# Kernel optimization log

Hardware: AMD Instinct MI355X
Metric: run time of the kernel (lower is better)

The kernel has to match this reference:

```python
import jax, jax.numpy as jnp
import numpy as np

B, S, D = 2, 2048, 2560
H, DH = 32, 80           # heads, head_size = D // H
RD = 32                  # rotary_dim (partial RoPE)
NI = 10240               # n_inner = 4 * n_embd
EPS = 1e-5
ROPE_BASE = 10000.0


def setup_inputs() -> dict:
    key = jax.random.key(0)
    ks = jax.random.split(key, 12)
    sd = 0.02
    inp = {
        "position_ids": jnp.broadcast_to(jnp.arange(S, dtype=jnp.int64), (B, S)),
        "hidden_states": jax.random.normal(ks[0], (B, S, D), jnp.float32),
        "ln_g": jnp.ones((D,), jnp.float32),
        "ln_b": jnp.zeros((D,), jnp.float32),
        "wqkv": jax.random.normal(ks[1], (D, 3 * D), jnp.float32) * sd,
        "bqkv": jnp.zeros((3 * D,), jnp.float32),
        "wout": jax.random.normal(ks[2], (D, D), jnp.float32) * sd,
        "bout": jnp.zeros((D,), jnp.float32),
        "wfc1": jax.random.normal(ks[3], (D, NI), jnp.float32) * sd,
        "bfc1": jnp.zeros((NI,), jnp.float32),
        "wfc2": jax.random.normal(ks[4], (NI, D), jnp.float32) * sd,
        "bfc2": jnp.zeros((D,), jnp.float32),
    }
    return inp


def _rope_neox(x, positions):
    # x: [B,S,H,DH]; apply neox-style rotary to first RD dims only
    half = RD // 2
    inv_freq = 1.0 / (ROPE_BASE ** (jnp.arange(0, RD, 2, dtype=jnp.float32) / RD))  # [half]
    ang = positions.astype(jnp.float32)[..., None] * inv_freq                        # [B,S,half]
    cos = jnp.cos(ang)[:, :, None, :]  # [B,S,1,half]
    sin = jnp.sin(ang)[:, :, None, :]
    x1 = x[..., :half]
    x2 = x[..., half:RD]
    rot = jnp.concatenate([x1 * cos - x2 * sin, x2 * cos + x1 * sin], axis=-1)
    return jnp.concatenate([rot, x[..., RD:]], axis=-1)


def reference(position_ids, hidden_states, ln_g, ln_b, wqkv, bqkv, wout, bout,
              wfc1, bfc1, wfc2, bfc2):
    residual = hidden_states
    # LayerNorm
    mu = jnp.mean(hidden_states, axis=-1, keepdims=True)
    var = jnp.mean(jnp.square(hidden_states - mu), axis=-1, keepdims=True)
    x = (hidden_states - mu) * jax.lax.rsqrt(var + EPS) * ln_g + ln_b

    # QKV projection
    qkv = x @ wqkv + bqkv
    q, k, v = jnp.split(qkv, 3, axis=-1)
    q = q.reshape(B, S, H, DH)
    k = k.reshape(B, S, H, DH)
    v = v.reshape(B, S, H, DH)

    # partial RoPE (neox style) on q and k
    q = _rope_neox(q, position_ids)
    k = _rope_neox(k, position_ids)

    # causal attention
    scale = DH ** -0.5
    scores = jnp.einsum("bqhd,bkhd->bhqk", q, k) * scale
    causal = jnp.tril(jnp.ones((S, S), jnp.bool_))
    scores = jnp.where(causal, scores, jnp.finfo(scores.dtype).min)
    probs = jax.nn.softmax(scores, axis=-1)
    attn = jnp.einsum("bhqk,bkhd->bqhd", probs, v).reshape(B, S, D)
    attn_out = attn @ wout + bout

    # MLP (gelu_new = tanh-approx gelu) on the SAME normed x (parallel residual)
    mlp = jax.nn.gelu(x @ wfc1 + bfc1, approximate=True) @ wfc2 + bfc2

    return attn_out + mlp + residual
```

## Files before the change

### kernel.cpp

```cpp
#include <hip/hip_runtime.h>

#define SS   2048
#define DD   2560
#define HH   32
#define DHH  80
#define DPAD 96
#define NII  10240
#define NTOK 4096

typedef __attribute__((ext_vector_type(8))) __bf16 bf16x8;
typedef __attribute__((ext_vector_type(4))) float  f32x4;

__device__ __forceinline__ float bf2f(unsigned short h) {
  union { unsigned u; float f; } c; c.u = ((unsigned)h) << 16; return c.f;
}
__device__ __forceinline__ unsigned short f2bf(float f) {
  union { float f; unsigned u; } c; c.f = f;
  unsigned r = c.u + 0x7FFFu + ((c.u >> 16) & 1u);
  return (unsigned short)(r >> 16);
}

__device__ __forceinline__ void gl_lds16(const void* gptr, void* lptr) {
  __builtin_amdgcn_global_load_lds((__attribute__((address_space(1))) void*)gptr,
                                   (__attribute__((address_space(3))) void*)lptr,
                                   16, 0, 0);
}

__global__ __launch_bounds__(256) void wt_transpose(const float* __restrict__ W,
                                                    unsigned short* __restrict__ Wt,
                                                    int K, int N) {
  __shared__ float tile[32][33];
  const int tx = threadIdx.x & 31, ty = threadIdx.x >> 5;
  const int n0 = blockIdx.x * 32, k0 = blockIdx.y * 32;
#pragma unroll
  for (int i = 0; i < 32; i += 8)
    tile[ty + i][tx] = W[(size_t)(k0 + ty + i) * N + n0 + tx];
  __syncthreads();
#pragma unroll
  for (int i = 0; i < 32; i += 8)
    Wt[(size_t)(n0 + ty + i) * K + k0 + tx] = f2bf(tile[tx][ty + i]);
}

__global__ __launch_bounds__(256) void ln_kernel(const float* __restrict__ X,
                                                 const float* __restrict__ G,
                                                 const float* __restrict__ Bb,
                                                 unsigned short* __restrict__ Xo) {
  const int row = blockIdx.x;
  const float4* xr = (const float4*)(X + (size_t)row * DD);
  float s = 0.f, ss = 0.f;
  for (int i = threadIdx.x; i < DD / 4; i += 256) {
    float4 v = xr[i];
    s  += v.x + v.y + v.z + v.w;
    ss += v.x * v.x + v.y * v.y + v.z * v.z + v.w * v.w;
  }
#pragma unroll
  for (int o = 32; o > 0; o >>= 1) { s += __shfl_down(s, o, 64); ss += __shfl_down(ss, o, 64); }
  __shared__ float red[8];
  const int w = threadIdx.x >> 6;
  if ((threadIdx.x & 63) == 0) { red[w] = s; red[4 + w] = ss; }
  __syncthreads();
  if (threadIdx.x == 0) {
    float ts  = red[0] + red[1] + red[2] + red[3];
    float tss = red[4] + red[5] + red[6] + red[7];
    float mu  = ts * (1.f / DD);
    float var = tss * (1.f / DD) - mu * mu;
    red[0] = mu; red[1] = rsqrtf(var + 1e-5f);
  }
  __syncthreads();
  const float mu = red[0], rstd = red[1];
  const float4* gr = (const float4*)G;
  const float4* br = (const float4*)Bb;
  for (int i = threadIdx.x; i < DD / 4; i += 256) {
    float4 v = xr[i], g = gr[i], b = br[i];
    ushort4 o;
    o.x = f2bf((v.x - mu) * rstd * g.x + b.x);
    o.y = f2bf((v.y - mu) * rstd * g.y + b.y);
    o.z = f2bf((v.z - mu) * rstd * g.z + b.z);
    o.w = f2bf((v.w - mu) * rstd * g.w + b.w);
    *(ushort4*)&Xo[(size_t)row * DD + i * 4] = o;
  }
}

__global__ __launch_bounds__(256) void rope_kernel(const unsigned short* __restrict__ qkv,
                                                   unsigned short* __restrict__ Qp,
                                                   unsigned short* __restrict__ Kp,
                                                   unsigned short* __restrict__ Vt) {
  const int tok = blockIdx.x;
  const int b = tok / SS, s = tok % SS;
  __shared__ float cs[16], sn[16];
  if (threadIdx.x < 16) {
    float inv = powf(10000.f, -(float)threadIdx.x / 16.f);
    float ang = (float)s * inv;
    cs[threadIdx.x] = cosf(ang);
    sn[threadIdx.x] = sinf(ang);
  }
  __syncthreads();
  const unsigned short* row = qkv + (size_t)tok * (3 * DD);
  for (int idx = threadIdx.x; idx < 2 * HH * DPAD; idx += 256) {
    const int which = idx / (HH * DPAD);
    const int rrem  = idx % (HH * DPAD);
    const int h = rrem / DPAD, d = rrem % DPAD;
    float val = 0.f;
    if (d < DHH) {
      const unsigned short* base = row + which * DD + h * DHH;
      if (d < 16) {
        float x1 = bf2f(base[d]), x2 = bf2f(base[d + 16]);
        val = x1 * cs[d] - x2 * sn[d];
      } else if (d < 32) {
        int i2 = d - 16;
        float x1 = bf2f(base[i2]), x2 = bf2f(base[d]);
        val = x2 * cs[i2] + x1 * sn[i2];
      } else {
        val = bf2f(base[d]);
      }
    }
    unsigned short* outp = which ? Kp : Qp;
    outp[(((size_t)b * HH + h) * SS + s) * DPAD + d] = f2bf(val);
  }
  for (int idx = threadIdx.x; idx < DD; idx += 256) {
    const int h = idx / DHH, d = idx % DHH;
    Vt[(((size_t)b * HH + h) * DHH + d) * SS + s] = row[2 * DD + idx];
  }
}

__global__ __launch_bounds__(128) void attn_kernel(const unsigned short* __restrict__ Qp,
                                                   const unsigned short* __restrict__ Kp,
                                                   const unsigned short* __restrict__ Vt,
                                                   unsigned short* __restrict__ O) {
  const int bid = blockIdx.x;
  const int bh = bid & 63;
  const int p = 63 - (bid >> 6);
  const int w = threadIdx.x >> 6;
  const int tile = p * 2 + w;
  const int lane = threadIdx.x & 63;
  const int lr = lane & 15, lg = lane >> 4;
  const int q0 = tile * 16;
  const unsigned short* Qh = Qp + (size_t)bh * SS * DPAD;
  const unsigned short* Kh = Kp + (size_t)bh * SS * DPAD;
  const unsigned short* Vh = Vt + (size_t)bh * DHH * SS;
  __shared__ __align__(16) char Plds[2][2048];
  char* Pb = Plds[w];

  bf16x8 qf[3];
#pragma unroll
  for (int c = 0; c < 3; ++c)
    qf[c] = *(const bf16x8*)&Qh[(size_t)(q0 + lr) * DPAD + c * 32 + lg * 8];

  f32x4 oacc[5];
#pragma unroll
  for (int d = 0; d < 5; ++d) oacc[d] = (f32x4){0.f, 0.f, 0.f, 0.f};
  float mrow[4], lrow[4];
#pragma unroll
  for (int r = 0; r < 4; ++r) { mrow[r] = -1e30f; lrow[r] = 0.f; }

  const float scl = 0.11180339887498949f;
  const int nt = q0 / 64 + 1;
  for (int t = 0; t < nt; ++t) {
    const int kv0 = t * 64;
    f32x4 s0 = (f32x4){0.f, 0.f, 0.f, 0.f};
    f32x4 s1 = (f32x4){0.f, 0.f, 0.f, 0.f};
    f32x4 s2 = (f32x4){0.f, 0.f, 0.f, 0.f};
    f32x4 s3 = (f32x4){0.f, 0.f, 0.f, 0.f};
#pragma unroll
    for (int c = 0; c < 3; ++c) {
      bf16x8 k0 = *(const bf16x8*)&Kh[(size_t)(kv0 +      lr) * DPAD + c * 32 + lg * 8];
      bf16x8 k1 = *(const bf16x8*)&Kh[(size_t)(kv0 + 16 + lr) * DPAD + c * 32 + lg * 8];
      bf16x8 k2 = *(const bf16x8*)&Kh[(size_t)(kv0 + 32 + lr) * DPAD + c * 32 + lg * 8];
      bf16x8 k3 = *(const bf16x8*)&Kh[(size_t)(kv0 + 48 + lr) * DPAD + c * 32 + lg * 8];
      s0 = __builtin_amdgcn_mfma_f32_16x16x32_bf16(qf[c], k0, s0, 0, 0, 0);
      s1 = __builtin_amdgcn_mfma_f32_16x16x32_bf16(qf[c], k1, s1, 0, 0, 0);
      s2 = __builtin_amdgcn_mfma_f32_16x16x32_bf16(qf[c], k2, s2, 0, 0, 0);
      s3 = __builtin_amdgcn_mfma_f32_16x16x32_bf16(qf[c], k3, s3, 0, 0, 0);
    }
    float pv0[4], pv1[4], pv2[4], pv3[4], mx[4];
    bool need = false;
#pragma unroll
    for (int r = 0; r < 4; ++r) {
      const int qr = q0 + lg * 4 + r;
      float a0 = (kv0 +      lr > qr) ? -1e30f : s0[r] * scl;
      float a1 = (kv0 + 16 + lr > qr) ? -1e30f : s1[r] * scl;
      float a2 = (kv0 + 32 + lr > qr) ? -1e30f : s2[r] * scl;
      float a3 = (kv0 + 48 + lr > qr) ? -1e30f : s3[r] * scl;
      pv0[r] = a0; pv1[r] = a1; pv2[r] = a2; pv3[r] = a3;
      float m = fmaxf(fmaxf(a0, a1), fmaxf(a2, a3));
#pragma unroll
      for (int mk = 1; mk < 16; mk <<= 1) m = fmaxf(m, __shfl_xor(m, mk, 64));
      mx[r] = m;
      need = need || (m > mrow[r] + 8.f);
    }
    if (__ballot(need)) {
#pragma unroll
      for (int r = 0; r < 4; ++r) {
        float mnew = fmaxf(mrow[r], mx[r]);
        float resc = __expf(mrow[r] - mnew);
        lrow[r] *= resc;
#pragma unroll
        for (int d = 0; d < 5; ++d) oacc[d][r] *= resc;
        mrow[r] = mnew;
      }
    }
#pragma unroll
    for (int r = 0; r < 4; ++r) {
      const int row = lg * 4 + r;
      const int swz = (row & 7) << 4;
      float p0 = __expf(pv0[r] - mrow[r]);
      float p1 = __expf(pv1[r] - mrow[r]);
      float p2 = __expf(pv2[r] - mrow[r]);
      float p3 = __expf(pv3[r] - mrow[r]);
      *(unsigned short*)(Pb + row * 128 + ((( 0 + lr) * 2) ^ swz)) = f2bf(p0);
      *(unsigned short*)(Pb + row * 128 + (((16 + lr) * 2) ^ swz)) = f2bf(p1);
      *(unsigned short*)(Pb + row * 128 + (((32 + lr) * 2) ^ swz)) = f2bf(p2);
      *(unsigned short*)(Pb + row * 128 + (((48 + lr) * 2) ^ swz)) = f2bf(p3);
      float rs = (p0 + p1) + (p2 + p3);
#pragma unroll
      for (int mk = 1; mk < 16; mk <<= 1) rs += __shfl_xor(rs, mk, 64);
      lrow[r] += rs;
    }
    asm volatile("s_waitcnt lgkmcnt(0)" ::: "memory");
    const int rswz = (lr & 7) << 4;
    bf16x8 pa0 = *(const bf16x8*)(Pb + lr * 128 + ((lg * 16) ^ rswz));
    bf16x8 pa1 = *(const bf16x8*)(Pb + lr * 128 + ((64 + lg * 16) ^ rswz));
#pragma unroll
    for (int d = 0; d < 5; ++d) {
      bf16x8 v0 = *(const bf16x8*)&Vh[(size_t)(d * 16 + lr) * SS + kv0 + lg * 8];
      bf16x8 v1 = *(const bf16x8*)&Vh[(size_t)(d * 16 + lr) * SS + kv0 + 32 + lg * 8];
      oacc[d] = __builtin_amdgcn_mfma_f32_16x16x32_bf16(pa0, v0, oacc[d], 0, 0, 0);
      oacc[d] = __builtin_amdgcn_mfma_f32_16x16x32_bf16(pa1, v1, oacc[d], 0, 0, 0);
    }
  }
  const int b = bh >> 5, h = bh & 31;
#pragma unroll
  for (int r = 0; r < 4; ++r) {
    const int qr = q0 + lg * 4 + r;
    const float inv = 1.f / lrow[r];
#pragma unroll
    for (int d = 0; d < 5; ++d)
      O[(size_t)(b * SS + qr) * DD + h * DHH + d * 16 + lr] = f2bf(oacc[d][r] * inv);
  }
}

__device__ __forceinline__ float gelu_f(float x) {
  float x3 = x * x * x;
  return 0.5f * x * (1.f + tanhf(0.7978845608028654f * (x + 0.044715f * x3)));
}

template <int MODE>
__global__ __launch_bounds__(512, 2) void gemm256(const unsigned short* __restrict__ A,
                                                  const unsigned short* __restrict__ Bt,
                                                  const float* __restrict__ bias,
                                                  void* __restrict__ Cout,
                                                  const unsigned short* __restrict__ addb,
                                                  const float* __restrict__ addf,
                                                  int M, int N, int K, int nbx) {
  __shared__ __align__(16) char lds[131072];

  const int nwg = gridDim.x;
  const int orig = blockIdx.x;
  const int qq = nwg >> 3, rr = nwg & 7;
  const int xcd = orig & 7, loc = orig >> 3;
  const int swz = (xcd < rr ? xcd * (qq + 1) : rr * (qq + 1) + (xcd - rr) * qq) + loc;
  const int by = swz / nbx, bx = swz % nbx;
  const int m0 = by * 256, n0 = bx * 256;

  const int tid = threadIdx.x;
  const int w = tid >> 6, lane = tid & 63;
  const int lr = lane & 15, lg = lane >> 4;
  const int wm = w & 1, wn = w >> 1;

  const int srow = w * 32 + (lane >> 2);
  const int skc  = ((lane & 3) ^ ((lane >> 3) & 3)) * 8;
  const unsigned short* aSrc = A  + (size_t)(m0 + srow) * K + skc;
  const unsigned short* bSrc = Bt + (size_t)(n0 + srow) * K + skc;
  const int sdst = w * 2048;

  const int fsw = (lg ^ ((lr >> 1) & 3)) << 4;
  const int arowb = (wm * 128 + lr) * 64;
  const int browb = (wn * 64 + lr) * 64;

  f32x4 acc[8][4];
#pragma unroll
  for (int i = 0; i < 8; ++i)
#pragma unroll
    for (int j = 0; j < 4; ++j) acc[i][j] = (f32x4){0.f, 0.f, 0.f, 0.f};

  const int nt = K >> 6;

#define STG(srcp, kt, h, base)                                          \
  { const unsigned short* _g = (srcp) + (size_t)(kt) * 64 + (h) * 32;   \
    gl_lds16(_g, lds + (base) + sdst);                                  \
    gl_lds16(_g + (size_t)16 * K, lds + (base) + sdst + 1024); }
#define LDAF(base, h, m) (*(const bf16x8*)(lds + (base) + (h) * 16384 + arowb + (m) * 1024 + fsw))
#define LDBF(base, h, n) (*(const bf16x8*)(lds + (base) + (h) * 16384 + browb + (n) * 1024 + fsw))
#define MFMA16(lo)                                                      \
  _Pragma("unroll") for (int i = 0; i < 4; ++i)                         \
  _Pragma("unroll") for (int j = 0; j < 4; ++j)                         \
    acc[(lo) + i][j] = __builtin_amdgcn_mfma_f32_16x16x32_bf16(av[i], bv[j], acc[(lo) + i][j], 0, 0, 0);

  STG(aSrc, 0, 0, 0);
  STG(bSrc, 0, 0, 65536);
  STG(aSrc, 0, 1, 16384);
  STG(bSrc, 0, 1, 65536 + 16384);
  STG(aSrc, 1, 0, 32768);
  STG(bSrc, 1, 0, 65536 + 32768);
  asm volatile("s_waitcnt vmcnt(4)" ::: "memory");
  __builtin_amdgcn_s_barrier();
  __builtin_amdgcn_sched_barrier(0);

  for (int k = 0; k < nt; ++k) {
    const int c = k & 1;
    const int cAb = c * 32768,         cBb = 65536 + c * 32768;
    const int nAb = (c ^ 1) * 32768,   nBb = 65536 + (c ^ 1) * 32768;
    bf16x8 av[4], bv[4];
#pragma unroll
    for (int i = 0; i < 4; ++i) av[i] = LDAF(cAb, 0, i);
#pragma unroll
    for (int j = 0; j < 4; ++j) bv[j] = LDBF(cBb, 0, j);
    if (k + 1 < nt) STG(aSrc, k + 1, 1, nAb + 16384);
    __builtin_amdgcn_s_barrier();
    __builtin_amdgcn_s_setprio(1);
    MFMA16(0);
    __builtin_amdgcn_s_setprio(0);
    __builtin_amdgcn_s_barrier();
#pragma unroll
    for (int i = 0; i < 4; ++i) av[i] = LDAF(cAb, 0, 4 + i);
    if (k + 1 < nt) STG(bSrc, k + 1, 1, nBb + 16384);
    __builtin_amdgcn_s_barrier();
    __builtin_amdgcn_s_setprio(1);
    MFMA16(4);
    __builtin_amdgcn_s_setprio(0);
    __builtin_amdgcn_s_barrier();
#pragma unroll
    for (int i = 0; i < 4; ++i) av[i] = LDAF(cAb, 1, i);
#pragma unroll
    for (int j = 0; j < 4; ++j) bv[j] = LDBF(cBb, 1, j);
    if (k + 2 < nt) STG(aSrc, k + 2, 0, cAb);
    __builtin_amdgcn_s_barrier();
    __builtin_amdgcn_s_setprio(1);
    MFMA16(0);
    __builtin_amdgcn_s_setprio(0);
    __builtin_amdgcn_s_barrier();
#pragma unroll
    for (int i = 0; i < 4; ++i) av[i] = LDAF(cAb, 1, 4 + i);
    if (k + 2 < nt) STG(bSrc, k + 2, 0, cBb);
    __builtin_amdgcn_s_barrier();
    __builtin_amdgcn_s_setprio(1);
    MFMA16(4);
    __builtin_amdgcn_s_setprio(0);
    const int rem = nt - 1 - k;
    if (rem >= 2) asm volatile("s_waitcnt vmcnt(4)" ::: "memory");
    else          asm volatile("s_waitcnt vmcnt(0)" ::: "memory");
    __builtin_amdgcn_s_barrier();
    __builtin_amdgcn_sched_barrier(0);
  }
#undef STG
#undef LDAF
#undef LDBF
#undef MFMA16

#pragma unroll
  for (int m = 0; m < 8; ++m) {
    const int rb = m0 + wm * 128 + m * 16 + lg * 4;
#pragma unroll
    for (int n = 0; n < 4; ++n) {
      const int col = n0 + wn * 64 + n * 16 + lr;
      const float bv = bias[col];
#pragma unroll
      for (int r = 0; r < 4; ++r) {
        const size_t idx = (size_t)(rb + r) * N + col;
        float v = acc[m][n][r] + bv;
        if (MODE == 2) v = gelu_f(v);
        if (MODE == 3) {
          ((float*)Cout)[idx] = v + bf2f(addb[idx]) + addf[idx];
        } else {
          ((unsigned short*)Cout)[idx] = f2bf(v);
        }
      }
    }
  }
}

extern "C" void kernel_launch(void* const* d_in, const int* in_sizes, int n_in,
                              void* d_out, int out_size, void* d_ws, size_t ws_size,
                              hipStream_t stream) {
  (void)in_sizes; (void)n_in; (void)out_size; (void)ws_size;
  const float* hidden = (const float*)d_in[1];
  const float* ln_g = (const float*)d_in[2];
  const float* ln_b = (const float*)d_in[3];
  const float* wqkv = (const float*)d_in[4];
  const float* bqkv = (const float*)d_in[5];
  const float* wout = (const float*)d_in[6];
  const float* bout = (const float*)d_in[7];
  const float* wfc1 = (const float*)d_in[8];
  const float* bfc1 = (const float*)d_in[9];
  const float* wfc2 = (const float*)d_in[10];
  const float* bfc2 = (const float*)d_in[11];
  float* out = (float*)d_out;

  char* ws = (char*)d_ws;
  size_t off = 0;
  auto alloc = [&](size_t bytes) -> void* {
    void* p = ws + off;
    off += (bytes + 255) & ~(size_t)255;
    return p;
  };
  unsigned short* wqkvT = (unsigned short*)alloc((size_t)3 * DD * DD * 2);
  unsigned short* woutT = (unsigned short*)alloc((size_t)DD * DD * 2);
  unsigned short* wfc1T = (unsigned short*)alloc((size_t)NII * DD * 2);
  unsigned short* wfc2T = (unsigned short*)alloc((size_t)DD * NII * 2);
  unsigned short* xln   = (unsigned short*)alloc((size_t)NTOK * DD * 2);
  unsigned short* regA  = (unsigned short*)alloc((size_t)NTOK * NII * 2);
  unsigned short* Qp    = (unsigned short*)alloc((size_t)2 * HH * SS * DPAD * 2);
  unsigned short* Kp    = (unsigned short*)alloc((size_t)2 * HH * SS * DPAD * 2);
  unsigned short* Vt    = (unsigned short*)alloc((size_t)2 * HH * DHH * SS * 2);
  unsigned short* Obuf  = (unsigned short*)alloc((size_t)NTOK * DD * 2);
  unsigned short* qkvbuf   = regA;
  unsigned short* h1       = regA;
  unsigned short* attnproj = Qp;

  wt_transpose<<<dim3(3 * DD / 32, DD / 32), 256, 0, stream>>>(wqkv, wqkvT, DD, 3 * DD);
  wt_transpose<<<dim3(DD / 32, DD / 32), 256, 0, stream>>>(wout, woutT, DD, DD);
  wt_transpose<<<dim3(NII / 32, DD / 32), 256, 0, stream>>>(wfc1, wfc1T, DD, NII);
  wt_transpose<<<dim3(DD / 32, NII / 32), 256, 0, stream>>>(wfc2, wfc2T, NII, DD);
  ln_kernel<<<NTOK, 256, 0, stream>>>(hidden, ln_g, ln_b, xln);
  gemm256<0><<<dim3((3 * DD / 256) * (NTOK / 256)), 512, 0, stream>>>(
      xln, wqkvT, bqkv, qkvbuf, nullptr, nullptr, NTOK, 3 * DD, DD, 3 * DD / 256);
  rope_kernel<<<NTOK, 256, 0, stream>>>(qkvbuf, Qp, Kp, Vt);
  attn_kernel<<<dim3(4096), 128, 0, stream>>>(Qp, Kp, Vt, Obuf);
  gemm256<0><<<dim3((DD / 256) * (NTOK / 256)), 512, 0, stream>>>(
      Obuf, woutT, bout, attnproj, nullptr, nullptr, NTOK, DD, DD, DD / 256);
  gemm256<2><<<dim3((NII / 256) * (NTOK / 256)), 512, 0, stream>>>(
      xln, wfc1T, bfc1, h1, nullptr, nullptr, NTOK, NII, DD, NII / 256);
  gemm256<3><<<dim3((DD / 256) * (NTOK / 256)), 512, 0, stream>>>(
      h1, wfc2T, bfc2, out, attnproj, hidden, NTOK, DD, NII, DD / 256);
}
```

Measured before the change: 1.313 ms.

## Replace 256x256 pipelined GEMM with simpler 128x128 double-buffered GEMM

Shrinks the GEMM tile from 256x256 with 512 threads to 128x128 with 256 threads, using a K step of 32 and a simple double-buffered LDS loop with one barrier per step. The aim is more workgroups, higher occupancy (4 blocks per CU) and less LDS per block. In exchange, each loaded byte is reused less, which raises global and LDS traffic. It also drops the fine-grained barrier and priority interleaving that hid load latency.

```diff
diff --git a/kernel.cpp b/kernel.cpp
--- a/kernel.cpp
+++ b/kernel.cpp
@@ -245,14 +245,14 @@
 }
 
 template <int MODE>
-__global__ __launch_bounds__(512, 2) void gemm256(const unsigned short* __restrict__ A,
+__global__ __launch_bounds__(256, 4) void gemm128(const unsigned short* __restrict__ A,
                                                   const unsigned short* __restrict__ Bt,
                                                   const float* __restrict__ bias,
                                                   void* __restrict__ Cout,
                                                   const unsigned short* __restrict__ addb,
                                                   const float* __restrict__ addf,
                                                   int M, int N, int K, int nbx) {
-  __shared__ __align__(16) char lds[131072];
+  __shared__ __align__(16) char lds[32768];
 
   const int nwg = gridDim.x;
   const int orig = blockIdx.x;
@@ -260,7 +260,7 @@
   const int xcd = orig & 7, loc = orig >> 3;
   const int swz = (xcd < rr ? xcd * (qq + 1) : rr * (qq + 1) + (xcd - rr) * qq) + loc;
   const int by = swz / nbx, bx = swz % nbx;
-  const int m0 = by * 256, n0 = bx * 256;
+  const int m0 = by * 128, n0 = bx * 128;
 
   const int tid = threadIdx.x;
   const int w = tid >> 6, lane = tid & 63;
@@ -274,92 +274,61 @@
   const int sdst = w * 2048;
 
   const int fsw = (lg ^ ((lr >> 1) & 3)) << 4;
-  const int arowb = (wm * 128 + lr) * 64;
+  const int arowb = (wm * 64 + lr) * 64;
   const int browb = (wn * 64 + lr) * 64;
 
-  f32x4 acc[8][4];
-#pragma unroll
-  for (int i = 0; i < 8; ++i)
+  f32x4 acc[4][4];
+#pragma unroll
+  for (int i = 0; i < 4; ++i)
 #pragma unroll
     for (int j = 0; j < 4; ++j) acc[i][j] = (f32x4){0.f, 0.f, 0.f, 0.f};
 
-  const int nt = K >> 6;
-
-#define STG(srcp, kt, h, base)                                          \
-  { const unsigned short* _g = (srcp) + (size_t)(kt) * 64 + (h) * 32;   \
-    gl_lds16(_g, lds + (base) + sdst);                                  \
-    gl_lds16(_g + (size_t)16 * K, lds + (base) + sdst + 1024); }
-#define LDAF(base, h, m) (*(const bf16x8*)(lds + (base) + (h) * 16384 + arowb + (m) * 1024 + fsw))
-#define LDBF(base, h, n) (*(const bf16x8*)(lds + (base) + (h) * 16384 + browb + (n) * 1024 + fsw))
-#define MFMA16(lo)                                                      \
-  _Pragma("unroll") for (int i = 0; i < 4; ++i)                         \
-  _Pragma("unroll") for (int j = 0; j < 4; ++j)                         \
-    acc[(lo) + i][j] = __builtin_amdgcn_mfma_f32_16x16x32_bf16(av[i], bv[j], acc[(lo) + i][j], 0, 0, 0);
-
-  STG(aSrc, 0, 0, 0);
-  STG(bSrc, 0, 0, 65536);
-  STG(aSrc, 0, 1, 16384);
-  STG(bSrc, 0, 1, 65536 + 16384);
-  STG(aSrc, 1, 0, 32768);
-  STG(bSrc, 1, 0, 65536 + 32768);
-  asm volatile("s_waitcnt vmcnt(4)" ::: "memory");
-  __builtin_amdgcn_s_barrier();
-  __builtin_amdgcn_sched_barrier(0);
-
-  for (int k = 0; k < nt; ++k) {
-    const int c = k & 1;
-    const int cAb = c * 32768,         cBb = 65536 + c * 32768;
-    const int nAb = (c ^ 1) * 32768,   nBb = 65536 + (c ^ 1) * 32768;
-    bf16x8 av[4], bv[4];
-#pragma unroll
-    for (int i = 0; i < 4; ++i) av[i] = LDAF(cAb, 0, i);
-#pragma unroll
-    for (int j = 0; j < 4; ++j) bv[j] = LDBF(cBb, 0, j);
-    if (k + 1 < nt) STG(aSrc, k + 1, 1, nAb + 16384);
-    __builtin_amdgcn_s_barrier();
-    __builtin_amdgcn_s_setprio(1);
-    MFMA16(0);
-    __builtin_amdgcn_s_setprio(0);
-    __builtin_amdgcn_s_barrier();
-#pragma unroll
-    for (int i = 0; i < 4; ++i) av[i] = LDAF(cAb, 0, 4 + i);
-    if (k + 1 < nt) STG(bSrc, k + 1, 1, nBb + 16384);
-    __builtin_amdgcn_s_barrier();
-    __builtin_amdgcn_s_setprio(1);
-    MFMA16(4);
-    __builtin_amdgcn_s_setprio(0);
-    __builtin_amdgcn_s_barrier();
-#pragma unroll
-    for (int i = 0; i < 4; ++i) av[i] = LDAF(cAb, 1, i);
-#pragma unroll
-    for (int j = 0; j < 4; ++j) bv[j] = LDBF(cBb, 1, j);
-    if (k + 2 < nt) STG(aSrc, k + 2, 0, cAb);
-    __builtin_amdgcn_s_barrier();
-    __builtin_amdgcn_s_setprio(1);
-    MFMA16(0);
-    __builtin_amdgcn_s_setprio(0);
-    __builtin_amdgcn_s_barrier();
-#pragma unroll
-    for (int i = 0; i < 4; ++i) av[i] = LDAF(cAb, 1, 4 + i);
-    if (k + 2 < nt) STG(bSrc, k + 2, 0, cBb);
-    __builtin_amdgcn_s_barrier();
-    __builtin_amdgcn_s_setprio(1);
-    MFMA16(4);
-    __builtin_amdgcn_s_setprio(0);
-    const int rem = nt - 1 - k;
-    if (rem >= 2) asm volatile("s_waitcnt vmcnt(4)" ::: "memory");
-    else          asm volatile("s_waitcnt vmcnt(0)" ::: "memory");
-    __builtin_amdgcn_s_barrier();
-    __builtin_amdgcn_sched_barrier(0);
-  }
-#undef STG
-#undef LDAF
-#undef LDBF
-#undef MFMA16
-
-#pragma unroll
-  for (int m = 0; m < 8; ++m) {
-    const int rb = m0 + wm * 128 + m * 16 + lg * 4;
+  const int nt = K >> 5;
+
+#define STAGE(t, b)                                                       \
+  { const unsigned short* _a = aSrc + (size_t)(t) * 32;                   \
+    const unsigned short* _b = bSrc + (size_t)(t) * 32;                   \
+    gl_lds16(_a,                lds + (b) * 8192 + sdst);                 \
+    gl_lds16(_a + (size_t)16 * K, lds + (b) * 8192 + sdst + 1024);        \
+    gl_lds16(_b,                lds + 16384 + (b) * 8192 + sdst);         \
+    gl_lds16(_b + (size_t)16 * K, lds + 16384 + (b) * 8192 + sdst + 1024); }
+#define LDA(b, m) (*(const bf16x8*)(lds + (b) * 8192 + arowb + (m) * 1024 + fsw))
+#define LDB(b, n) (*(const bf16x8*)(lds + 16384 + (b) * 8192 + browb + (n) * 1024 + fsw))
+
+  STAGE(0, 0);
+  __syncthreads();
+
+  for (int t = 0; t < nt; ++t) {
+    const int cur = t & 1;
+    if (t + 1 < nt) STAGE(t + 1, cur ^ 1);
+    bf16x8 bv0 = LDB(cur, 0), bv1 = LDB(cur, 1), bv2 = LDB(cur, 2), bv3 = LDB(cur, 3);
+    bf16x8 a0 = LDA(cur, 0), a1 = LDA(cur, 1);
+    acc[0][0] = __builtin_amdgcn_mfma_f32_16x16x32_bf16(a0, bv0, acc[0][0], 0, 0, 0);
+    acc[0][1] = __builtin_amdgcn_mfma_f32_16x16x32_bf16(a0, bv1, acc[0][1], 0, 0, 0);
+    acc[0][2] = __builtin_amdgcn_mfma_f32_16x16x32_bf16(a0, bv2, acc[0][2], 0, 0, 0);
+    acc[0][3] = __builtin_amdgcn_mfma_f32_16x16x32_bf16(a0, bv3, acc[0][3], 0, 0, 0);
+    acc[1][0] = __builtin_amdgcn_mfma_f32_16x16x32_bf16(a1, bv0, acc[1][0], 0, 0, 0);
+    acc[1][1] = __builtin_amdgcn_mfma_f32_16x16x32_bf16(a1, bv1, acc[1][1], 0, 0, 0);
+    acc[1][2] = __builtin_amdgcn_mfma_f32_16x16x32_bf16(a1, bv2, acc[1][2], 0, 0, 0);
+    acc[1][3] = __builtin_amdgcn_mfma_f32_16x16x32_bf16(a1, bv3, acc[1][3], 0, 0, 0);
+    bf16x8 a2 = LDA(cur, 2), a3 = LDA(cur, 3);
+    acc[2][0] = __builtin_amdgcn_mfma_f32_16x16x32_bf16(a2, bv0, acc[2][0], 0, 0, 0);
+    acc[2][1] = __builtin_amdgcn_mfma_f32_16x16x32_bf16(a2, bv1, acc[2][1], 0, 0, 0);
+    acc[2][2] = __builtin_amdgcn_mfma_f32_16x16x32_bf16(a2, bv2, acc[2][2], 0, 0, 0);
+    acc[2][3] = __builtin_amdgcn_mfma_f32_16x16x32_bf16(a2, bv3, acc[2][3], 0, 0, 0);
+    acc[3][0] = __builtin_amdgcn_mfma_f32_16x16x32_bf16(a3, bv0, acc[3][0], 0, 0, 0);
+    acc[3][1] = __builtin_amdgcn_mfma_f32_16x16x32_bf16(a3, bv1, acc[3][1], 0, 0, 0);
+    acc[3][2] = __builtin_amdgcn_mfma_f32_16x16x32_bf16(a3, bv2, acc[3][2], 0, 0, 0);
+    acc[3][3] = __builtin_amdgcn_mfma_f32_16x16x32_bf16(a3, bv3, acc[3][3], 0, 0, 0);
+    __syncthreads();
+  }
+#undef STAGE
+#undef LDA
+#undef LDB
+
+#pragma unroll
+  for (int m = 0; m < 4; ++m) {
+    const int rb = m0 + wm * 64 + m * 16 + lg * 4;
 #pragma unroll
     for (int n = 0; n < 4; ++n) {
       const int col = n0 + wn * 64 + n * 16 + lr;
@@ -422,14 +391,14 @@
   wt_transpose<<<dim3(NII / 32, DD / 32), 256, 0, stream>>>(wfc1, wfc1T, DD, NII);
   wt_transpose<<<dim3(DD / 32, NII / 32), 256, 0, stream>>>(wfc2, wfc2T, NII, DD);
   ln_kernel<<<NTOK, 256, 0, stream>>>(hidden, ln_g, ln_b, xln);
-  gemm256<0><<<dim3((3 * DD / 256) * (NTOK / 256)), 512, 0, stream>>>(
-      xln, wqkvT, bqkv, qkvbuf, nullptr, nullptr, NTOK, 3 * DD, DD, 3 * DD / 256);
+  gemm128<0><<<dim3((3 * DD / 128) * (NTOK / 128)), 256, 0, stream>>>(
+      xln, wqkvT, bqkv, qkvbuf, nullptr, nullptr, NTOK, 3 * DD, DD, 3 * DD / 128);
   rope_kernel<<<NTOK, 256, 0, stream>>>(qkvbuf, Qp, Kp, Vt);
   attn_kernel<<<dim3(4096), 128, 0, stream>>>(Qp, Kp, Vt, Obuf);
-  gemm256<0><<<dim3((DD / 256) * (NTOK / 256)), 512, 0, stream>>>(
-      Obuf, woutT, bout, attnproj, nullptr, nullptr, NTOK, DD, DD, DD / 256);
-  gemm256<2><<<dim3((NII / 256) * (NTOK / 256)), 512, 0, stream>>>(
-      xln, wfc1T, bfc1, h1, nullptr, nullptr, NTOK, NII, DD, NII / 256);
-  gemm256<3><<<dim3((DD / 256) * (NTOK / 256)), 512, 0, stream>>>(
-      h1, wfc2T, bfc2, out, attnproj, hidden, NTOK, DD, NII, DD / 256);
-}
+  gemm128<0><<<dim3((DD / 128) * (NTOK / 128)), 256, 0, stream>>>(
+      Obuf, woutT, bout, attnproj, nullptr, nullptr, NTOK, DD, DD, DD / 128);
+  gemm128<2><<<dim3((NII / 128) * (NTOK / 128)), 256, 0, stream>>>(
+      xln, wfc1T, bfc1, h1, nullptr, nullptr, NTOK, NII, DD, NII / 128);
+  gemm128<3><<<dim3((DD / 128) * (NTOK / 128)), 256, 0, stream>>>(
+      h1, wfc2T, bfc2, out, attnproj, hidden, NTOK, DD, NII, DD / 128);
+}
```

Result: slower. 1.344 ms (+2.4%).

## Restructure GEMM main loop with 64-wide k tiles and 4x2 wave layout

Applied to the files above, without the earlier changes.

Rewrites the bf16 GEMM inner loop to stage whole 64-wide k tiles into a double-buffered LDS layout with an XOR swizzle over 8 chunks. Waves are remapped from a 2x4 to a 4-column grid, and each step runs four MFMA phases that reuse A and B fragments across sub-tiles. Loads for the next tile are issued during the current tile's compute, and every step ends with a full vmcnt(0) wait. This changes the prefetch depth, so load latency may be less hidden than with the earlier partial-wait scheme. The A fragments for rows 4-7 are read from LDS twice per step.

```diff
diff --git a/kernel.cpp b/kernel.cpp
--- a/kernel.cpp
+++ b/kernel.cpp
@@ -265,17 +265,18 @@
   const int tid = threadIdx.x;
   const int w = tid >> 6, lane = tid & 63;
   const int lr = lane & 15, lg = lane >> 4;
-  const int wm = w & 1, wn = w >> 1;
-
-  const int srow = w * 32 + (lane >> 2);
-  const int skc  = ((lane & 3) ^ ((lane >> 3) & 3)) * 8;
-  const unsigned short* aSrc = A  + (size_t)(m0 + srow) * K + skc;
-  const unsigned short* bSrc = Bt + (size_t)(n0 + srow) * K + skc;
-  const int sdst = w * 2048;
-
-  const int fsw = (lg ^ ((lr >> 1) & 3)) << 4;
-  const int arowb = (wm * 128 + lr) * 64;
-  const int browb = (wn * 64 + lr) * 64;
+  const int wm = w >> 2, wn = w & 3;
+
+  const int l8 = lane >> 3, l7 = lane & 7;
+  const unsigned short* aStg = A  + (size_t)(m0 + w * 32 + l8) * K + ((l7 ^ l8) * 8);
+  const unsigned short* bStg = Bt + (size_t)(n0 + w * 32 + l8) * K + ((l7 ^ l8) * 8);
+  const int stgDst = w * 4096;
+
+  const int s0 = lg ^ (lr & 7);
+  const int a0 = (wm * 128 + lr) * 128 + (s0 << 4);
+  const int a1 = (wm * 128 + lr) * 128 + ((s0 << 4) ^ 64);
+  const int b0 = (wn * 64 + lr) * 128 + (s0 << 4);
+  const int b1 = (wn * 64 + lr) * 128 + ((s0 << 4) ^ 64);
 
   f32x4 acc[8][4];
 #pragma unroll
@@ -283,79 +284,88 @@
 #pragma unroll
     for (int j = 0; j < 4; ++j) acc[i][j] = (f32x4){0.f, 0.f, 0.f, 0.f};
 
-  const int nt = K >> 6;
-
-#define STG(srcp, kt, h, base)                                          \
-  { const unsigned short* _g = (srcp) + (size_t)(kt) * 64 + (h) * 32;   \
-    gl_lds16(_g, lds + (base) + sdst);                                  \
-    gl_lds16(_g + (size_t)16 * K, lds + (base) + sdst + 1024); }
-#define LDAF(base, h, m) (*(const bf16x8*)(lds + (base) + (h) * 16384 + arowb + (m) * 1024 + fsw))
-#define LDBF(base, h, n) (*(const bf16x8*)(lds + (base) + (h) * 16384 + browb + (n) * 1024 + fsw))
-#define MFMA16(lo)                                                      \
-  _Pragma("unroll") for (int i = 0; i < 4; ++i)                         \
-  _Pragma("unroll") for (int j = 0; j < 4; ++j)                         \
-    acc[(lo) + i][j] = __builtin_amdgcn_mfma_f32_16x16x32_bf16(av[i], bv[j], acc[(lo) + i][j], 0, 0, 0);
-
-  STG(aSrc, 0, 0, 0);
-  STG(bSrc, 0, 0, 65536);
-  STG(aSrc, 0, 1, 16384);
-  STG(bSrc, 0, 1, 65536 + 16384);
-  STG(aSrc, 1, 0, 32768);
-  STG(bSrc, 1, 0, 65536 + 32768);
-  asm volatile("s_waitcnt vmcnt(4)" ::: "memory");
+  const int nsteps = K >> 6;
+
+#define STGA(DST, i) gl_lds16(aStg + (size_t)(i) * 8 * K, lds + (DST) + stgDst + (i) * 1024)
+#define STGB(DST, i) gl_lds16(bStg + (size_t)(i) * 8 * K, lds + 65536 + (DST) + stgDst + (i) * 1024)
+#define RDA(CUR, m, kh) (*(const bf16x8*)(lds + (CUR) + (m) * 2048 + ((kh) ? a1 : a0)))
+#define RDB(CUR, n, kh) (*(const bf16x8*)(lds + 65536 + (CUR) + (n) * 2048 + ((kh) ? b1 : b0)))
+
+#define GSTEP(CUR, NXT, scur)                                                            \
+  {                                                                                      \
+    const bool stg = (scur) + 1 < nsteps;                                                \
+    bf16x8 av[4][2], bv0[2][2];                                                          \
+    _Pragma("unroll") for (int m = 0; m < 4; ++m) {                                      \
+      av[m][0] = RDA(CUR, m, 0); av[m][1] = RDA(CUR, m, 1); }                            \
+    _Pragma("unroll") for (int n = 0; n < 2; ++n) {                                      \
+      bv0[n][0] = RDB(CUR, n, 0); bv0[n][1] = RDB(CUR, n, 1); }                          \
+    if (stg) { STGA(NXT, 0); STGA(NXT, 1); STGA(NXT, 2); STGA(NXT, 3); }                 \
+    __builtin_amdgcn_s_barrier();                                                        \
+    __builtin_amdgcn_s_setprio(1);                                                       \
+    _Pragma("unroll") for (int kh = 0; kh < 2; ++kh)                                     \
+    _Pragma("unroll") for (int m = 0; m < 4; ++m)                                        \
+    _Pragma("unroll") for (int n = 0; n < 2; ++n)                                        \
+      acc[m][n] = __builtin_amdgcn_mfma_f32_16x16x32_bf16(av[m][kh], bv0[n][kh],         \
+                                                          acc[m][n], 0, 0, 0);           \
+    __builtin_amdgcn_s_setprio(0);                                                       \
+    __builtin_amdgcn_s_barrier();                                                        \
+    bf16x8 av2[4][2];                                                                    \
+    _Pragma("unroll") for (int m = 0; m < 4; ++m) {                                      \
+      av2[m][0] = RDA(CUR, 4 + m, 0); av2[m][1] = RDA(CUR, 4 + m, 1); }                  \
+    if (stg) { STGB(NXT, 0); STGB(NXT, 1); STGB(NXT, 2); STGB(NXT, 3); }                 \
+    __builtin_amdgcn_s_barrier();                                                        \
+    __builtin_amdgcn_s_setprio(1);                                                       \
+    _Pragma("unroll") for (int kh = 0; kh < 2; ++kh)                                     \
+    _Pragma("unroll") for (int m = 0; m < 4; ++m)                                        \
+    _Pragma("unroll") for (int n = 0; n < 2; ++n)                                        \
+      acc[4 + m][n] = __builtin_amdgcn_mfma_f32_16x16x32_bf16(av2[m][kh], bv0[n][kh],    \
+                                                              acc[4 + m][n], 0, 0, 0);   \
+    __builtin_amdgcn_s_setprio(0);                                                       \
+    __builtin_amdgcn_s_barrier();                                                        \
+    bf16x8 bv1[2][2];                                                                    \
+    _Pragma("unroll") for (int n = 0; n < 2; ++n) {                                      \
+      bv1[n][0] = RDB(CUR, 2 + n, 0); bv1[n][1] = RDB(CUR, 2 + n, 1); }                  \
+    __builtin_amdgcn_s_barrier();                                                        \
+    __builtin_amdgcn_s_setprio(1);                                                       \
+    _Pragma("unroll") for (int kh = 0; kh < 2; ++kh)                                     \
+    _Pragma("unroll") for (int m = 0; m < 4; ++m)                                        \
+    _Pragma("unroll") for (int n = 0; n < 2; ++n)                                        \
+      acc[m][2 + n] = __builtin_amdgcn_mfma_f32_16x16x32_bf16(av[m][kh], bv1[n][kh],     \
+                                                              acc[m][2 + n], 0, 0, 0);   \
+    __builtin_amdgcn_s_setprio(0);                                                       \
+    __builtin_amdgcn_s_barrier();                                                        \
+    _Pragma("unroll") for (int m = 0; m < 4; ++m) {                                      \
+      av2[m][0] = RDA(CUR, 4 + m, 0); av2[m][1] = RDA(CUR, 4 + m, 1); }                  \
+    __builtin_amdgcn_s_barrier();                                                        \
+    __builtin_amdgcn_s_setprio(1);                                                       \
+    _Pragma("unroll") for (int kh = 0; kh < 2; ++kh)                                     \
+    _Pragma("unroll") for (int m = 0; m < 4; ++m)                                        \
+    _Pragma("unroll") for (int n = 0; n < 2; ++n)                                        \
+      acc[4 + m][2 + n] = __builtin_amdgcn_mfma_f32_16x16x32_bf16(av2[m][kh],            \
+                                          bv1[n][kh], acc[4 + m][2 + n], 0, 0, 0);       \
+    __builtin_amdgcn_s_setprio(0);                                                       \
+    asm volatile("s_waitcnt vmcnt(0)" ::: "memory");                                     \
+    __builtin_amdgcn_s_barrier();                                                        \
+    __builtin_amdgcn_sched_barrier(0);                                                   \
+    aStg += 64; bStg += 64;                                                              \
+  }
+
+  STGA(0, 0); STGA(0, 1); STGA(0, 2); STGA(0, 3);
+  STGB(0, 0); STGB(0, 1); STGB(0, 2); STGB(0, 3);
+  aStg += 64; bStg += 64;
+  asm volatile("s_waitcnt vmcnt(0)" ::: "memory");
   __builtin_amdgcn_s_barrier();
   __builtin_amdgcn_sched_barrier(0);
 
-  for (int k = 0; k < nt; ++k) {
-    const int c = k & 1;
-    const int cAb = c * 32768,         cBb = 65536 + c * 32768;
-    const int nAb = (c ^ 1) * 32768,   nBb = 65536 + (c ^ 1) * 32768;
-    bf16x8 av[4], bv[4];
-#pragma unroll
-    for (int i = 0; i < 4; ++i) av[i] = LDAF(cAb, 0, i);
-#pragma unroll
-    for (int j = 0; j < 4; ++j) bv[j] = LDBF(cBb, 0, j);
-    if (k + 1 < nt) STG(aSrc, k + 1, 1, nAb + 16384);
-    __builtin_amdgcn_s_barrier();
-    __builtin_amdgcn_s_setprio(1);
-    MFMA16(0);
-    __builtin_amdgcn_s_setprio(0);
-    __builtin_amdgcn_s_barrier();
-#pragma unroll
-    for (int i = 0; i < 4; ++i) av[i] = LDAF(cAb, 0, 4 + i);
-    if (k + 1 < nt) STG(bSrc, k + 1, 1, nBb + 16384);
-    __builtin_amdgcn_s_barrier();
-    __builtin_amdgcn_s_setprio(1);
-    MFMA16(4);
-    __builtin_amdgcn_s_setprio(0);
-    __builtin_amdgcn_s_barrier();
-#pragma unroll
-    for (int i = 0; i < 4; ++i) av[i] = LDAF(cAb, 1, i);
-#pragma unroll
-    for (int j = 0; j < 4; ++j) bv[j] = LDBF(cBb, 1, j);
-    if (k + 2 < nt) STG(aSrc, k + 2, 0, cAb);
-    __builtin_amdgcn_s_barrier();
-    __builtin_amdgcn_s_setprio(1);
-    MFMA16(0);
-    __builtin_amdgcn_s_setprio(0);
-    __builtin_amdgcn_s_barrier();
-#pragma unroll
-    for (int i = 0; i < 4; ++i) av[i] = LDAF(cAb, 1, 4 + i);
-    if (k + 2 < nt) STG(bSrc, k + 2, 0, cBb);
-    __builtin_amdgcn_s_barrier();
-    __builtin_amdgcn_s_setprio(1);
-    MFMA16(4);
-    __builtin_amdgcn_s_setprio(0);
-    const int rem = nt - 1 - k;
-    if (rem >= 2) asm volatile("s_waitcnt vmcnt(4)" ::: "memory");
-    else          asm volatile("s_waitcnt vmcnt(0)" ::: "memory");
-    __builtin_amdgcn_s_barrier();
-    __builtin_amdgcn_sched_barrier(0);
-  }
-#undef STG
-#undef LDAF
-#undef LDBF
-#undef MFMA16
+  for (int s = 0; s < nsteps; s += 2) {
+    GSTEP(0, 32768, s);
+    GSTEP(32768, 0, s + 1);
+  }
+#undef GSTEP
+#undef STGA
+#undef STGB
+#undef RDA
+#undef RDB
 
 #pragma unroll
   for (int m = 0; m < 8; ++m) {
```

Result: no change. 1.334 ms (+1.6%).

## Restructure GEMM main loop into 8-phase ping-pong schedule with 128B swizzled LDS rows

Applied to the files above, without the earlier changes.

Rewrites the bf16 GEMM mainloop. Each LDS row now holds a full 64-wide K tile (128 bytes) with an 8-way XOR swizzle, and the wave-to-tile mapping changes. The loop is unrolled over two K tiles, and each quadrant is computed as an 8x2 MFMA block with A and B fragments reused across quadrants. Global-to-LDS stages are interleaved between barriers with explicit lgkmcnt waits. The goal is fewer LDS reads per MFMA and better overlap of loads with matrix math, at the cost of more barriers, more register pressure and schedule fragility. It assumes an even number of K tiles.

```diff
diff --git a/kernel.cpp b/kernel.cpp
--- a/kernel.cpp
+++ b/kernel.cpp
@@ -265,17 +265,18 @@
   const int tid = threadIdx.x;
   const int w = tid >> 6, lane = tid & 63;
   const int lr = lane & 15, lg = lane >> 4;
-  const int wm = w & 1, wn = w >> 1;
-
-  const int srow = w * 32 + (lane >> 2);
-  const int skc  = ((lane & 3) ^ ((lane >> 3) & 3)) * 8;
-  const unsigned short* aSrc = A  + (size_t)(m0 + srow) * K + skc;
-  const unsigned short* bSrc = Bt + (size_t)(n0 + srow) * K + skc;
-  const int sdst = w * 2048;
-
-  const int fsw = (lg ^ ((lr >> 1) & 3)) << 4;
-  const int arowb = (wm * 128 + lr) * 64;
-  const int browb = (wn * 64 + lr) * 64;
+  const int wm = w >> 2, wn = w & 3;
+
+  const int srow = w * 16 + (lane >> 3);
+  const int scol = ((lane & 7) ^ ((lane >> 3) & 7)) * 8;
+  const unsigned short* pA = A  + (size_t)(m0 + srow) * K + scol;
+  const unsigned short* pB = Bt + (size_t)(n0 + srow) * K + scol;
+  const int wdst = w * 2048;
+
+  const int rdA = wm * 16384 + lr * 128;
+  const int rdB = 65536 + (wn >> 1) * 16384 + ((wn & 1) * 64 + lr) * 128;
+  const int sl0 = ((lg) ^ (lr & 7)) << 4;
+  const int sl1 = ((4 + lg) ^ (lr & 7)) << 4;
 
   f32x4 acc[8][4];
 #pragma unroll
@@ -285,77 +286,105 @@
 
   const int nt = K >> 6;
 
-#define STG(srcp, kt, h, base)                                          \
-  { const unsigned short* _g = (srcp) + (size_t)(kt) * 64 + (h) * 32;   \
-    gl_lds16(_g, lds + (base) + sdst);                                  \
-    gl_lds16(_g + (size_t)16 * K, lds + (base) + sdst + 1024); }
-#define LDAF(base, h, m) (*(const bf16x8*)(lds + (base) + (h) * 16384 + arowb + (m) * 1024 + fsw))
-#define LDBF(base, h, n) (*(const bf16x8*)(lds + (base) + (h) * 16384 + browb + (n) * 1024 + fsw))
-#define MFMA16(lo)                                                      \
-  _Pragma("unroll") for (int i = 0; i < 4; ++i)                         \
-  _Pragma("unroll") for (int j = 0; j < 4; ++j)                         \
-    acc[(lo) + i][j] = __builtin_amdgcn_mfma_f32_16x16x32_bf16(av[i], bv[j], acc[(lo) + i][j], 0, 0, 0);
-
-  STG(aSrc, 0, 0, 0);
-  STG(bSrc, 0, 0, 65536);
-  STG(aSrc, 0, 1, 16384);
-  STG(bSrc, 0, 1, 65536 + 16384);
-  STG(aSrc, 1, 0, 32768);
-  STG(bSrc, 1, 0, 65536 + 32768);
-  asm volatile("s_waitcnt vmcnt(4)" ::: "memory");
-  __builtin_amdgcn_s_barrier();
+#define RA(BUF, m, kh) (*(const bf16x8*)(lds + (BUF) + rdA + (m) * 2048 + ((kh) ? sl1 : sl0)))
+#define RB(BUF, n, kh) (*(const bf16x8*)(lds + (BUF) + rdB + (n) * 2048 + ((kh) ? sl1 : sl0)))
+#define STGA(dt, h, DST)                                                       \
+  { const unsigned short* s_ = pA + (size_t)(dt) * 64 + (size_t)(h) * 128 * K; \
+    gl_lds16(s_,                 lds + (DST) + wdst);                          \
+    gl_lds16(s_ + (size_t)8 * K, lds + (DST) + wdst + 1024); }
+#define STGB(dt, h, DST)                                                       \
+  { const unsigned short* s_ = pB + (size_t)(dt) * 64 + (size_t)(h) * 128 * K; \
+    gl_lds16(s_,                 lds + 65536 + (DST) + wdst);                  \
+    gl_lds16(s_ + (size_t)8 * K, lds + 65536 + (DST) + wdst + 1024); }
+#define BARR __builtin_amdgcn_s_barrier()
+#define LGKM0 { asm volatile("s_waitcnt lgkmcnt(0)" ::: "memory"); __builtin_amdgcn_sched_barrier(0); }
+#define MFMA8x2(AV, BV, MB, NB)                                              \
+  __builtin_amdgcn_s_setprio(1);                                             \
+  _Pragma("unroll") for (int kh_ = 0; kh_ < 2; ++kh_)                        \
+  _Pragma("unroll") for (int m_ = 0; m_ < 4; ++m_)                           \
+  _Pragma("unroll") for (int n_ = 0; n_ < 2; ++n_)                           \
+    acc[(MB) + m_][(NB) + n_] = __builtin_amdgcn_mfma_f32_16x16x32_bf16(     \
+        AV[m_][kh_], BV[n_][kh_], acc[(MB) + m_][(NB) + n_], 0, 0, 0);       \
+  __builtin_amdgcn_s_setprio(0);
+
+  STGA(0, 0, 0);
+  STGA(0, 1, 16384);
+  STGB(0, 0, 0);
+  STGB(0, 1, 16384);
+  STGA(1, 0, 32768);
+  STGA(1, 1, 32768 + 16384);
+  STGB(1, 0, 32768);
+  asm volatile("s_waitcnt vmcnt(6)" ::: "memory");
+  BARR;
   __builtin_amdgcn_sched_barrier(0);
 
-  for (int k = 0; k < nt; ++k) {
-    const int c = k & 1;
-    const int cAb = c * 32768,         cBb = 65536 + c * 32768;
-    const int nAb = (c ^ 1) * 32768,   nBb = 65536 + (c ^ 1) * 32768;
-    bf16x8 av[4], bv[4];
-#pragma unroll
-    for (int i = 0; i < 4; ++i) av[i] = LDAF(cAb, 0, i);
-#pragma unroll
-    for (int j = 0; j < 4; ++j) bv[j] = LDBF(cBb, 0, j);
-    if (k + 1 < nt) STG(aSrc, k + 1, 1, nAb + 16384);
-    __builtin_amdgcn_s_barrier();
-    __builtin_amdgcn_s_setprio(1);
-    MFMA16(0);
-    __builtin_amdgcn_s_setprio(0);
-    __builtin_amdgcn_s_barrier();
-#pragma unroll
-    for (int i = 0; i < 4; ++i) av[i] = LDAF(cAb, 0, 4 + i);
-    if (k + 1 < nt) STG(bSrc, k + 1, 1, nBb + 16384);
-    __builtin_amdgcn_s_barrier();
-    __builtin_amdgcn_s_setprio(1);
-    MFMA16(4);
-    __builtin_amdgcn_s_setprio(0);
-    __builtin_amdgcn_s_barrier();
-#pragma unroll
-    for (int i = 0; i < 4; ++i) av[i] = LDAF(cAb, 1, i);
-#pragma unroll
-    for (int j = 0; j < 4; ++j) bv[j] = LDBF(cBb, 1, j);
-    if (k + 2 < nt) STG(aSrc, k + 2, 0, cAb);
-    __builtin_amdgcn_s_barrier();
-    __builtin_amdgcn_s_setprio(1);
-    MFMA16(0);
-    __builtin_amdgcn_s_setprio(0);
-    __builtin_amdgcn_s_barrier();
-#pragma unroll
-    for (int i = 0; i < 4; ++i) av[i] = LDAF(cAb, 1, 4 + i);
-    if (k + 2 < nt) STG(bSrc, k + 2, 0, cBb);
-    __builtin_amdgcn_s_barrier();
-    __builtin_amdgcn_s_setprio(1);
-    MFMA16(4);
-    __builtin_amdgcn_s_setprio(0);
-    const int rem = nt - 1 - k;
-    if (rem >= 2) asm volatile("s_waitcnt vmcnt(4)" ::: "memory");
-    else          asm volatile("s_waitcnt vmcnt(0)" ::: "memory");
-    __builtin_amdgcn_s_barrier();
+  for (int t = 0; t < nt; t += 2) {
+    const bool more = (t + 2 < nt);
+    bf16x8 avL[4][2], avH[4][2], bvL[2][2], bvH[2][2];
+
+#pragma unroll
+    for (int m_ = 0; m_ < 4; ++m_) { avL[m_][0] = RA(0, m_, 0); avL[m_][1] = RA(0, m_, 1); }
+#pragma unroll
+    for (int n_ = 0; n_ < 2; ++n_) { bvL[n_][0] = RB(0, n_, 0); bvL[n_][1] = RB(0, n_, 1); }
+    STGB(1, 1, 32768 + 16384);
+    BARR; LGKM0;
+    MFMA8x2(avL, bvL, 0, 0);
+    BARR;
+#pragma unroll
+    for (int m_ = 0; m_ < 4; ++m_) { avH[m_][0] = RA(0, 4 + m_, 0); avH[m_][1] = RA(0, 4 + m_, 1); }
+    BARR; LGKM0;
+    MFMA8x2(avH, bvL, 4, 0);
+    BARR;
+#pragma unroll
+    for (int n_ = 0; n_ < 2; ++n_) { bvH[n_][0] = RB(0, 2 + n_, 0); bvH[n_][1] = RB(0, 2 + n_, 1); }
+    if (more) STGA(2, 0, 0);
+    BARR; LGKM0;
+    MFMA8x2(avH, bvH, 4, 2);
+    BARR;
+    if (more) STGA(2, 1, 16384);
+    BARR;
+    MFMA8x2(avL, bvH, 0, 2);
+    if (more) { asm volatile("s_waitcnt vmcnt(4)" ::: "memory"); }
+    else      { asm volatile("s_waitcnt vmcnt(0)" ::: "memory"); }
+    BARR;
     __builtin_amdgcn_sched_barrier(0);
-  }
-#undef STG
-#undef LDAF
-#undef LDBF
-#undef MFMA16
+
+#pragma unroll
+    for (int m_ = 0; m_ < 4; ++m_) { avL[m_][0] = RA(32768, m_, 0); avL[m_][1] = RA(32768, m_, 1); }
+#pragma unroll
+    for (int n_ = 0; n_ < 2; ++n_) { bvL[n_][0] = RB(32768, n_, 0); bvL[n_][1] = RB(32768, n_, 1); }
+    if (more) STGB(2, 0, 0);
+    BARR; LGKM0;
+    MFMA8x2(avL, bvL, 0, 0);
+    BARR;
+#pragma unroll
+    for (int m_ = 0; m_ < 4; ++m_) { avH[m_][0] = RA(32768, 4 + m_, 0); avH[m_][1] = RA(32768, 4 + m_, 1); }
+    if (more) STGB(2, 1, 16384);
+    BARR; LGKM0;
+    MFMA8x2(avH, bvL, 4, 0);
+    BARR;
+#pragma unroll
+    for (int n_ = 0; n_ < 2; ++n_) { bvH[n_][0] = RB(32768, 2 + n_, 0); bvH[n_][1] = RB(32768, 2 + n_, 1); }
+    if (more) STGA(3, 0, 32768);
+    BARR; LGKM0;
+    MFMA8x2(avH, bvH, 4, 2);
+    BARR;
+    if (more) { STGA(3, 1, 32768 + 16384); STGB(3, 0, 32768); }
+    BARR;
+    MFMA8x2(avL, bvH, 0, 2);
+    if (more) { asm volatile("s_waitcnt vmcnt(6)" ::: "memory"); }
+    BARR;
+    __builtin_amdgcn_sched_barrier(0);
+
+    pA += 128; pB += 128;
+  }
+#undef RA
+#undef RB
+#undef STGA
+#undef STGB
+#undef BARR
+#undef LGKM0
+#undef MFMA8x2
 
 #pragma unroll
   for (int m = 0; m < 8; ++m) {
```

Result: no change. 1.308 ms (-0.3%).
